# Optimization experiments

Measured on AMD Instinct MI355X. Metric: run time of the kernel, lower is better.

Reference implementation:

```python
import jax, jax.numpy as jnp
import numpy as np

N_NEIGHBORS = 16
N_CLASSES = 10

def setup_inputs() -> dict:
    key = jax.random.key(0)
    k1, k2, k3 = jax.random.split(key, 3)
    x = jax.random.normal(k1, (1024, 64), dtype=jnp.float32)
    train_data = jax.random.normal(k2, (100000, 64), dtype=jnp.float32)
    train_labels = jax.random.randint(k3, (100000,), 0, N_CLASSES, dtype=jnp.int64)
    return {"x": x, "train_data": train_data, "train_labels": train_labels}

def reference(x, train_data, train_labels):
    # Pairwise L2 distances [B, N] via the quadratic expansion (same math as cdist p=2)
    x2 = jnp.sum(x * x, axis=-1, keepdims=True)            # [B, 1]
    t2 = jnp.sum(train_data * train_data, axis=-1)          # [N]
    d2 = x2 - 2.0 * (x @ train_data.T) + t2                 # [B, N]
    dist = jnp.sqrt(jnp.maximum(d2, 0.0))
    # k smallest distances
    neg_d, idx = jax.lax.top_k(-dist, N_NEIGHBORS)           # [B, k]
    d = -neg_d
    labels = train_labels[idx]                               # [B, k] gather
    # weights = 'distance': inverse distance, with exact-match rows handled
    w = 1.0 / d
    inf_mask = jnp.isinf(w)
    inf_row = jnp.any(inf_mask, axis=1, keepdims=True)
    w = jnp.where(inf_row, inf_mask.astype(w.dtype), w)
    # scatter_add weighted votes into [B, C]
    B = x.shape[0]
    rows = jnp.arange(B)[:, None]
    proba = jnp.zeros((B, N_CLASSES), dtype=w.dtype).at[rows, labels].add(w)
    s = jnp.sum(proba, axis=1, keepdims=True)
    s = jnp.where(s == 0.0, jnp.float32(1.0), s)
    proba = proba / s
    return jnp.argmax(proba, axis=1), proba
```

## Files before the change

### kernel.cpp

```cpp
#include <hip/hip_runtime.h>
#include <math.h>


constexpr int D        = 64;
constexpr int K        = 16;
constexpr int NCLS     = 10;
constexpr int CHUNKLEN = 896;
constexpr int NCHUNK   = 112;
constexpr int NPAD     = NCHUNK * CHUNKLEN + 32;
constexpr int NSUB     = 64;
constexpr int SUBLEN   = 128;
constexpr int SLOT     = 16;
constexpr int MSEL     = 48;

typedef __attribute__((ext_vector_type(8))) short bf16x8_t;
typedef __attribute__((ext_vector_type(4))) float f32x4_t;
typedef unsigned short ushort_t;

__device__ __forceinline__ ushort_t f32_to_bf16_rne(float f) {
  unsigned int u = __float_as_uint(f);
  unsigned int r = u + 0x7FFFu + ((u >> 16) & 1u);
  return (ushort_t)(r >> 16);
}

__device__ __forceinline__ bf16x8_t pack_bf16x8(float4 a, float4 b) {
  union { ushort_t u[8]; bf16x8_t v; } r;
  r.u[0] = f32_to_bf16_rne(a.x); r.u[1] = f32_to_bf16_rne(a.y);
  r.u[2] = f32_to_bf16_rne(a.z); r.u[3] = f32_to_bf16_rne(a.w);
  r.u[4] = f32_to_bf16_rne(b.x); r.u[5] = f32_to_bf16_rne(b.y);
  r.u[6] = f32_to_bf16_rne(b.z); r.u[7] = f32_to_bf16_rne(b.w);
  return r.v;
}

__global__ __launch_bounds__(256) void cvt_train(
    const float* __restrict__ t, ushort_t* __restrict__ tb,
    float* __restrict__ t2, float* __restrict__ nt2h, int N)
{
  int gid = blockIdx.x * 256 + threadIdx.x;
  int row = gid >> 2, qt = gid & 3;
  if (row >= NPAD) return;
  ushort_t* dst = tb + (size_t)row * D + qt * 16;
  if (row >= N) {
    uint2 z = make_uint2(0u, 0u);
    #pragma unroll
    for (int i = 0; i < 4; ++i) *reinterpret_cast<uint2*>(dst + i * 4) = z;
    if (qt == 0) { t2[row] = INFINITY; nt2h[row] = -INFINITY; }
    return;
  }
  const float* src = t + (size_t)row * D + qt * 16;
  float nrm = 0.f;
  #pragma unroll
  for (int i = 0; i < 4; ++i) {
    float4 v = *reinterpret_cast<const float4*>(src + i * 4);
    nrm = fmaf(v.x, v.x, nrm); nrm = fmaf(v.y, v.y, nrm);
    nrm = fmaf(v.z, v.z, nrm); nrm = fmaf(v.w, v.w, nrm);
    uint2 hh = make_uint2(
      (unsigned)f32_to_bf16_rne(v.x) | ((unsigned)f32_to_bf16_rne(v.y) << 16),
      (unsigned)f32_to_bf16_rne(v.z) | ((unsigned)f32_to_bf16_rne(v.w) << 16));
    *reinterpret_cast<uint2*>(dst + i * 4) = hh;
  }
  nrm += __shfl_xor(nrm, 1);
  nrm += __shfl_xor(nrm, 2);
  if (qt == 0) { t2[row] = nrm; nt2h[row] = -0.5f * nrm; }
}

__global__ __launch_bounds__(256) void knn_sample(
    const ushort_t* __restrict__ tb, const float* __restrict__ x,
    const float* __restrict__ nt2h, float* __restrict__ samp)
{
  const int tid = threadIdx.x;
  const int w = tid >> 6, lane = tid & 63;
  const int lh = lane & 15, lg = lane >> 4;
  const int qb = blockIdx.x, sub = blockIdx.y;
  const int q = qb * 64 + w * 16 + lh;

  const float* xrp = x + (size_t)q * D + lg * 8;
  bf16x8_t B0 = pack_bf16x8(*reinterpret_cast<const float4*>(xrp),
                            *reinterpret_cast<const float4*>(xrp + 4));
  bf16x8_t B1 = pack_bf16x8(*reinterpret_cast<const float4*>(xrp + 32),
                            *reinterpret_cast<const float4*>(xrp + 36));

  float Ld[4] = {-INFINITY, -INFINITY, -INFINITY, -INFINITY};

  const int pstart = sub * SUBLEN;
  const ushort_t* abase = tb + (size_t)pstart * D + lh * D + lg * 8;
  const float* nbase = nt2h + pstart + lg * 4;

  bf16x8_t A0[4], A1[4]; float4 NH[4];
  #pragma unroll
  for (int j = 0; j < 4; ++j) {
    const ushort_t* ap = abase + (size_t)j * 16 * D;
    A0[j] = *reinterpret_cast<const bf16x8_t*>(ap);
    A1[j] = *reinterpret_cast<const bf16x8_t*>(ap + 32);
    NH[j] = *reinterpret_cast<const float4*>(nbase + j * 16);
  }
  bf16x8_t N0[4], N1[4]; float4 NN[4];
  #pragma unroll
  for (int j = 0; j < 4; ++j) {
    const ushort_t* ap = abase + (size_t)(4 + j) * 16 * D;
    N0[j] = *reinterpret_cast<const bf16x8_t*>(ap);
    N1[j] = *reinterpret_cast<const bf16x8_t*>(ap + 32);
    NN[j] = *reinterpret_cast<const float4*>(nbase + (4 + j) * 16);
  }

  #pragma unroll
  for (int j = 0; j < 4; ++j) {
    f32x4_t c = {NH[j].x, NH[j].y, NH[j].z, NH[j].w};
    c = __builtin_amdgcn_mfma_f32_16x16x32_bf16(A0[j], B0, c, 0, 0, 0);
    c = __builtin_amdgcn_mfma_f32_16x16x32_bf16(A1[j], B1, c, 0, 0, 0);
    #pragma unroll
    for (int r = 0; r < 4; ++r) {
      float sv = c[r];
      if (sv > Ld[3]) {
        Ld[3] = sv;
        if (Ld[3] > Ld[2]) { float s_ = Ld[3]; Ld[3] = Ld[2]; Ld[2] = s_; }
        if (Ld[2] > Ld[1]) { float s_ = Ld[2]; Ld[2] = Ld[1]; Ld[1] = s_; }
        if (Ld[1] > Ld[0]) { float s_ = Ld[1]; Ld[1] = Ld[0]; Ld[0] = s_; }
      }
    }
  }
  #pragma unroll
  for (int j = 0; j < 4; ++j) {
    f32x4_t c = {NN[j].x, NN[j].y, NN[j].z, NN[j].w};
    c = __builtin_amdgcn_mfma_f32_16x16x32_bf16(N0[j], B0, c, 0, 0, 0);
    c = __builtin_amdgcn_mfma_f32_16x16x32_bf16(N1[j], B1, c, 0, 0, 0);
    #pragma unroll
    for (int r = 0; r < 4; ++r) {
      float sv = c[r];
      if (sv > Ld[3]) {
        Ld[3] = sv;
        if (Ld[3] > Ld[2]) { float s_ = Ld[3]; Ld[3] = Ld[2]; Ld[2] = s_; }
        if (Ld[2] > Ld[1]) { float s_ = Ld[2]; Ld[2] = Ld[1]; Ld[1] = s_; }
        if (Ld[1] > Ld[0]) { float s_ = Ld[1]; Ld[1] = Ld[0]; Ld[0] = s_; }
      }
    }
  }

  float* outp = samp + (size_t)q * (NSUB * 16) + sub * 16 + lg * 4;
  *reinterpret_cast<float4*>(outp) = make_float4(Ld[0], Ld[1], Ld[2], Ld[3]);
}

__global__ __launch_bounds__(256) void knn_theta(
    const float* __restrict__ samp, float* __restrict__ theta, int B)
{
  const int w = threadIdx.x >> 6, lane = threadIdx.x & 63;
  const int q = blockIdx.x * 4 + w;
  if (q >= B) return;

  const float* s = samp + (size_t)q * (NSUB * 16) + lane * 16;
  float4 p0 = *reinterpret_cast<const float4*>(s);
  float4 p1 = *reinterpret_cast<const float4*>(s + 4);
  float4 p2 = *reinterpret_cast<const float4*>(s + 8);
  float4 p3 = *reinterpret_cast<const float4*>(s + 12);
  float L0[4] = {p0.x, p0.y, p0.z, p0.w};
  float L1[4] = {p1.x, p1.y, p1.z, p1.w};
  float L2[4] = {p2.x, p2.y, p2.z, p2.w};
  float L3[4] = {p3.x, p3.y, p3.z, p3.w};

  float th = -INFINITY;
  for (int r = 0; r < K; ++r) {
    float bd = fmaxf(fmaxf(L0[0], L1[0]), fmaxf(L2[0], L3[0]));
    #pragma unroll
    for (int sdx = 0; sdx < 6; ++sdx) bd = fmaxf(bd, __shfl_xor(bd, 32 >> sdx));
    if (L0[0] == bd) { L0[0] = L0[1]; L0[1] = L0[2]; L0[2] = L0[3]; L0[3] = -INFINITY; }
    if (L1[0] == bd) { L1[0] = L1[1]; L1[1] = L1[2]; L1[2] = L1[3]; L1[3] = -INFINITY; }
    if (L2[0] == bd) { L2[0] = L2[1]; L2[1] = L2[2]; L2[2] = L2[3]; L2[3] = -INFINITY; }
    if (L3[0] == bd) { L3[0] = L3[1]; L3[1] = L3[2]; L3[2] = L3[3]; L3[3] = -INFINITY; }
    th = bd;
  }
  if (lane == 0) theta[q] = th;
}

__global__ __launch_bounds__(256) void knn_filter(
    const ushort_t* __restrict__ tb, const float* __restrict__ x,
    const float* __restrict__ nt2h, const float* __restrict__ theta,
    int* __restrict__ cnts, int2* __restrict__ cand2)
{
  __shared__ int  cnt_l[64];
  __shared__ int2 list_p[64][SLOT];

  const int tid = threadIdx.x;
  const int w = tid >> 6, lane = tid & 63;
  const int lh = lane & 15, lg = lane >> 4;

  const int d   = blockIdx.x + 16 * blockIdx.y;
  const int xcd = d & 7;
  const int t_  = d >> 3;
  const int qb  = t_ & 15;
  const int ch  = ((t_ >> 4) << 3) | xcd;

  const int q0 = qb * 64;
  const int wp0 = ch * CHUNKLEN + w * (CHUNKLEN / 4);

  if (tid < 64) cnt_l[tid] = 0;
  __syncthreads();

  bf16x8_t Bq0[4], Bq1[4];
  float th[4];
  #pragma unroll
  for (int ct = 0; ct < 4; ++ct) {
    const float* xrp = x + (size_t)(q0 + ct * 16 + lh) * D + lg * 8;
    Bq0[ct] = pack_bf16x8(*reinterpret_cast<const float4*>(xrp),
                          *reinterpret_cast<const float4*>(xrp + 4));
    Bq1[ct] = pack_bf16x8(*reinterpret_cast<const float4*>(xrp + 32),
                          *reinterpret_cast<const float4*>(xrp + 36));
    th[ct] = theta[q0 + ct * 16 + lh];
  }

  const ushort_t* abase = tb + (size_t)wp0 * D + lh * D + lg * 8;
  const float* nbase = nt2h + wp0 + lg * 4;

  bf16x8_t cA0 = *reinterpret_cast<const bf16x8_t*>(abase);
  bf16x8_t cA1 = *reinterpret_cast<const bf16x8_t*>(abase + 32);
  float4   cNA = *reinterpret_cast<const float4*>(nbase);
  bf16x8_t cB0 = *reinterpret_cast<const bf16x8_t*>(abase + (size_t)16 * D);
  bf16x8_t cB1 = *reinterpret_cast<const bf16x8_t*>(abase + (size_t)16 * D + 32);
  float4   cNB = *reinterpret_cast<const float4*>(nbase + 16);

  #define PROCESS(A0_, A1_, NH_, GIDX_)                                           \
    {                                                                             \
      const int pg = wp0 + (GIDX_) * 16 + lg * 4;                                 \
      _Pragma("unroll")                                                           \
      for (int ct = 0; ct < 4; ++ct) {                                            \
        f32x4_t c = {NH_.x, NH_.y, NH_.z, NH_.w};                                 \
        c = __builtin_amdgcn_mfma_f32_16x16x32_bf16(A0_, Bq0[ct], c, 0, 0, 0);    \
        c = __builtin_amdgcn_mfma_f32_16x16x32_bf16(A1_, Bq1[ct], c, 0, 0, 0);    \
        unsigned m = (c[0] >= th[ct] ? 1u : 0u) | (c[1] >= th[ct] ? 2u : 0u)      \
                   | (c[2] >= th[ct] ? 4u : 0u) | (c[3] >= th[ct] ? 8u : 0u);     \
        if (m) {                                                                  \
          const int qloc = ct * 16 + lh;                                          \
          int n = __popc(m);                                                      \
          int base = atomicAdd(&cnt_l[qloc], n);                                  \
          while (m) {                                                             \
            int r = __ffs(m) - 1; m &= m - 1;                                     \
            float sv = (r == 0) ? c[0] : (r == 1) ? c[1] : (r == 2) ? c[2] : c[3];\
            if (base < SLOT)                                                      \
              list_p[qloc][base] = make_int2(pg + r, __float_as_int(sv));         \
            ++base;                                                               \
          }                                                                       \
        }                                                                         \
      }                                                                           \
    }

  for (int g = 0; g < 7; ++g) {
    const ushort_t* an = abase + (size_t)(2 * g + 2) * 16 * D;
    bf16x8_t nA0 = *reinterpret_cast<const bf16x8_t*>(an);
    bf16x8_t nA1 = *reinterpret_cast<const bf16x8_t*>(an + 32);
    float4   nNA = *reinterpret_cast<const float4*>(nbase + (2 * g + 2) * 16);
    bf16x8_t nB0 = *reinterpret_cast<const bf16x8_t*>(an + (size_t)16 * D);
    bf16x8_t nB1 = *reinterpret_cast<const bf16x8_t*>(an + (size_t)16 * D + 32);
    float4   nNB = *reinterpret_cast<const float4*>(nbase + (2 * g + 3) * 16);

    PROCESS(cA0, cA1, cNA, 2 * g);
    PROCESS(cB0, cB1, cNB, 2 * g + 1);

    cA0 = nA0; cA1 = nA1; cNA = nNA;
    cB0 = nB0; cB1 = nB1; cNB = nNB;
  }
  #undef PROCESS

  __syncthreads();
  if (tid < 64) {
    int n = cnt_l[tid]; if (n > SLOT) n = SLOT;
    size_t o = (size_t)(q0 + tid) * NCHUNK + ch;
    cnts[o] = n;
    for (int j = 0; j < n; ++j) cand2[o * SLOT + j] = list_p[tid][j];
  }
}

__global__ __launch_bounds__(256) void knn_vote(
    const float* __restrict__ x, const float* __restrict__ train,
    const float* __restrict__ t2, const int* __restrict__ labels,
    const int* __restrict__ cnts, const int2* __restrict__ cand2,
    float* __restrict__ out, int B, int N)
{
  __shared__ int2  cpair[NCHUNK * SLOT];
  __shared__ float sortd[MSEL];
  __shared__ int   sorti[MSEL];
  __shared__ float xs[D];
  __shared__ int   total_s;
  __shared__ float x2_s;

  const int tid = threadIdx.x;
  const int w = tid >> 6, lane = tid & 63;
  const int q = blockIdx.x;

  if (tid == 0) total_s = 0;
  if (tid < D) xs[tid] = x[(size_t)q * D + tid];
  if (tid < MSEL) { sortd[tid] = INFINITY; sorti[tid] = 0x7fffffff; }
  __syncthreads();

  if (w == 0) {
    float v = xs[lane];
    float s = v * v;
    #pragma unroll
    for (int o = 32; o > 0; o >>= 1) s += __shfl_xor(s, o);
    if (lane == 0) x2_s = s;
  }
  if (tid < NCHUNK) {
    int n = cnts[(size_t)q * NCHUNK + tid];
    int base = atomicAdd(&total_s, n);
    const int2* src = cand2 + ((size_t)q * NCHUNK + tid) * SLOT;
    for (int j = 0; j < n; ++j) cpair[base + j] = src[j];
  }
  __syncthreads();

  const int total = total_s;
  const float x2 = x2_s;

  for (int j = tid; j < total; j += 256) {
    int2 mine = cpair[j];
    float ms = __int_as_float(mine.y);
    int   mi = mine.x;
    int rank = 0;
    for (int k = 0; k < total; ++k) {
      int2 o = cpair[k];
      float os = __int_as_float(o.y);
      rank += (os > ms || (os == ms && o.x < mi)) ? 1 : 0;
    }
    if (rank < MSEL) { sortd[rank] = ms; sorti[rank] = mi; }
  }
  __syncthreads();

  if (tid < MSEL) {
    int idx = sorti[tid];
    float d2v = INFINITY;
    if (idx != 0x7fffffff) {
      const float* tr = train + (size_t)idx * D;
      float dot = 0.f;
      #pragma unroll
      for (int i = 0; i < 16; ++i) {
        float4 tv = *reinterpret_cast<const float4*>(tr + i * 4);
        dot = fmaf(xs[i * 4 + 0], tv.x, dot); dot = fmaf(xs[i * 4 + 1], tv.y, dot);
        dot = fmaf(xs[i * 4 + 2], tv.z, dot); dot = fmaf(xs[i * 4 + 3], tv.w, dot);
      }
      d2v = fmaxf(x2 - 2.f * dot + t2[idx], 0.f);
    }
    sortd[tid] = d2v;
  }
  __syncthreads();

  if (w == 0) {
    float vd = (lane < MSEL) ? sortd[lane] : INFINITY;
    int   vi = (lane < MSEL) ? sorti[lane] : 0x7fffffff;
    float myD = INFINITY; int myI = 0;
    for (int r = 0; r < K; ++r) {
      float bd = vd; int bi = vi;
      #pragma unroll
      for (int s = 0; s < 6; ++s) {
        int off = 32 >> s;
        float od = __shfl_xor(bd, off);
        int   oi = __shfl_xor(bi, off);
        if (od < bd || (od == bd && oi < bi)) { bd = od; bi = oi; }
      }
      if (vd == bd && vi == bi) { vd = INFINITY; vi = 0x7fffffff; }
      if (lane == r) { myD = bd; myI = bi; }
    }

    int valid = (lane < K) && (myD < INFINITY) && (myI < N);
    float dist = sqrtf(fmaxf(myD, 0.f));
    int lab = labels[(valid && myI < N) ? myI : 0];
    int isz = (valid && dist == 0.f) ? 1 : 0;
    float wgt = 1.f / dist;

    float accw[NCLS]; float acci[NCLS]; int anyInf = 0;
    #pragma unroll
    for (int c = 0; c < NCLS; ++c) { accw[c] = 0.f; acci[c] = 0.f; }
    for (int r = 0; r < K; ++r) {
      int   vr   = __shfl(valid, r);
      int   labr = __shfl(lab, r);
      float wgtr = __shfl(wgt, r);
      int   iszr = __shfl(isz, r);
      if (vr) {
        anyInf |= iszr;
        #pragma unroll
        for (int c = 0; c < NCLS; ++c) {
          accw[c] += (labr == c) ? wgtr : 0.f;
          acci[c] += (labr == c && iszr) ? 1.f : 0.f;
        }
      }
    }

    if (lane == 0) {
      float proba[NCLS]; float s = 0.f;
      #pragma unroll
      for (int c = 0; c < NCLS; ++c) { proba[c] = anyInf ? acci[c] : accw[c]; s += proba[c]; }
      if (s == 0.f) s = 1.f;
      #pragma unroll
      for (int c = 0; c < NCLS; ++c) proba[c] = proba[c] / s;
      int best = 0; float bv = proba[0];
      #pragma unroll
      for (int c = 1; c < NCLS; ++c) if (proba[c] > bv) { bv = proba[c]; best = c; }
      out[q] = (float)best;
      #pragma unroll
      for (int c = 0; c < NCLS; ++c) out[B + q * NCLS + c] = proba[c];
    }
  }
}

extern "C" void kernel_launch(void* const* d_in, const int* in_sizes, int n_in,
                              void* d_out, int out_size, void* d_ws, size_t ws_size,
                              hipStream_t stream)
{
  const float* x      = (const float*)d_in[0];
  const float* train  = (const float*)d_in[1];
  const int*   labels = (const int*)d_in[2];
  float* out = (float*)d_out;

  const int B = in_sizes[0] / D;
  const int N = in_sizes[2];

  char* ws = (char*)d_ws;
  size_t off = 0;
  ushort_t* train_bf = (ushort_t*)(ws + off); off += (size_t)NPAD * D * 2;
  float*    t2       = (float*)(ws + off);    off += (size_t)NPAD * 4;
  float*    nt2h     = (float*)(ws + off);    off += (size_t)NPAD * 4;
  float*    theta    = (float*)(ws + off);    off += (size_t)B * 4;
  int*      cnts     = (int*)(ws + off);      off += (size_t)B * NCHUNK * 4;
  int2*     cand2    = (int2*)(ws + off);     off += (size_t)B * NCHUNK * SLOT * 8;
  float*    samp     = (float*)cand2;

  cvt_train<<<(NPAD * 4 + 255) / 256, 256, 0, stream>>>(train, train_bf, t2, nt2h, N);
  knn_sample<<<dim3(B / 64, NSUB), 256, 0, stream>>>(train_bf, x, nt2h, samp);
  knn_theta<<<(B + 3) / 4, 256, 0, stream>>>(samp, theta, B);
  knn_filter<<<dim3(16, NCHUNK), 256, 0, stream>>>(train_bf, x, nt2h, theta, cnts, cand2);
  knn_vote<<<B, 256, 0, stream>>>(x, train, t2, labels, cnts, cand2, out, B, N);
}
```

Baseline: 116.8 us.

## Simplify candidate filtering, unroll rank loop, split rescoring dot across lanes

In the scan kernel, the per-element threshold bitmask is replaced by a max-of-four early test followed by per-element atomicAdd insertion, making the common no-hit path cheaper at the cost of more atomics on hits. The vote kernel pads the candidate list to a multiple of four with sentinel entries and unrolls the rank-counting loop by four, which raises instruction-level parallelism. The exact fp32 rescoring of the 48 selected candidates now spreads each 64-element dot product over four lanes and combines them with shuffles, so each thread does less serial work.

```diff
diff --git a/kernel.cpp b/kernel.cpp
--- a/kernel.cpp
+++ b/kernel.cpp
@@ -219,24 +219,22 @@
 
   #define PROCESS(A0_, A1_, NH_, GIDX_)                                           \
     {                                                                             \
-      const int pg = wp0 + (GIDX_) * 16 + lg * 4;                                 \
       _Pragma("unroll")                                                           \
       for (int ct = 0; ct < 4; ++ct) {                                            \
         f32x4_t c = {NH_.x, NH_.y, NH_.z, NH_.w};                                 \
         c = __builtin_amdgcn_mfma_f32_16x16x32_bf16(A0_, Bq0[ct], c, 0, 0, 0);    \
         c = __builtin_amdgcn_mfma_f32_16x16x32_bf16(A1_, Bq1[ct], c, 0, 0, 0);    \
-        unsigned m = (c[0] >= th[ct] ? 1u : 0u) | (c[1] >= th[ct] ? 2u : 0u)      \
-                   | (c[2] >= th[ct] ? 4u : 0u) | (c[3] >= th[ct] ? 8u : 0u);     \
-        if (m) {                                                                  \
+        float mx = fmaxf(fmaxf(c[0], c[1]), fmaxf(c[2], c[3]));                   \
+        if (mx >= th[ct]) {                         \
           const int qloc = ct * 16 + lh;                                          \
-          int n = __popc(m);                                                      \
-          int base = atomicAdd(&cnt_l[qloc], n);                                  \
-          while (m) {                                                             \
-            int r = __ffs(m) - 1; m &= m - 1;                                     \
-            float sv = (r == 0) ? c[0] : (r == 1) ? c[1] : (r == 2) ? c[2] : c[3];\
-            if (base < SLOT)                                                      \
-              list_p[qloc][base] = make_int2(pg + r, __float_as_int(sv));         \
-            ++base;                                                               \
+          const int pg = wp0 + (GIDX_) * 16 + lg * 4;                             \
+          _Pragma("unroll")                                                       \
+          for (int r = 0; r < 4; ++r) {                                           \
+            if (c[r] >= th[ct]) {                                                 \
+              int pos = atomicAdd(&cnt_l[qloc], 1);                               \
+              if (pos < SLOT)                                                     \
+                list_p[qloc][pos] = make_int2(pg + r, __float_as_int(c[r]));      \
+            }                                                                     \
           }                                                                       \
         }                                                                         \
       }                                                                           \
@@ -274,7 +272,7 @@
     const int* __restrict__ cnts, const int2* __restrict__ cand2,
     float* __restrict__ out, int B, int N)
 {
-  __shared__ int2  cpair[NCHUNK * SLOT];
+  __shared__ int2  cpair[NCHUNK * SLOT + 4];
   __shared__ float sortd[MSEL];
   __shared__ int   sorti[MSEL];
   __shared__ float xs[D];
@@ -306,37 +304,51 @@
   __syncthreads();
 
   const int total = total_s;
+  const int totalPad = (total + 3) & ~3;
   const float x2 = x2_s;
+  if (tid < totalPad - total)
+    cpair[total + tid] = make_int2(0x7fffffff, __float_as_int(-INFINITY));
+  __syncthreads();
 
   for (int j = tid; j < total; j += 256) {
     int2 mine = cpair[j];
     float ms = __int_as_float(mine.y);
     int   mi = mine.x;
     int rank = 0;
-    for (int k = 0; k < total; ++k) {
-      int2 o = cpair[k];
-      float os = __int_as_float(o.y);
-      rank += (os > ms || (os == ms && o.x < mi)) ? 1 : 0;
+    for (int k = 0; k < totalPad; k += 4) {
+      int2 o0 = cpair[k];     int2 o1 = cpair[k + 1];
+      int2 o2 = cpair[k + 2]; int2 o3 = cpair[k + 3];
+      float s0 = __int_as_float(o0.y), s1 = __int_as_float(o1.y);
+      float s2 = __int_as_float(o2.y), s3 = __int_as_float(o3.y);
+      rank += ((s0 > ms || (s0 == ms && o0.x < mi)) ? 1 : 0)
+            + ((s1 > ms || (s1 == ms && o1.x < mi)) ? 1 : 0)
+            + ((s2 > ms || (s2 == ms && o2.x < mi)) ? 1 : 0)
+            + ((s3 > ms || (s3 == ms && o3.x < mi)) ? 1 : 0);
     }
     if (rank < MSEL) { sortd[rank] = ms; sorti[rank] = mi; }
   }
   __syncthreads();
 
-  if (tid < MSEL) {
-    int idx = sorti[tid];
-    float d2v = INFINITY;
+  if (tid < MSEL * 4) {
+    const int ci = tid >> 2, qt = tid & 3;
+    const int idx = sorti[ci];
+    float dot = 0.f;
     if (idx != 0x7fffffff) {
-      const float* tr = train + (size_t)idx * D;
-      float dot = 0.f;
-      #pragma unroll
-      for (int i = 0; i < 16; ++i) {
+      const float* tr = train + (size_t)idx * D + qt * 16;
+      #pragma unroll
+      for (int i = 0; i < 4; ++i) {
         float4 tv = *reinterpret_cast<const float4*>(tr + i * 4);
-        dot = fmaf(xs[i * 4 + 0], tv.x, dot); dot = fmaf(xs[i * 4 + 1], tv.y, dot);
-        dot = fmaf(xs[i * 4 + 2], tv.z, dot); dot = fmaf(xs[i * 4 + 3], tv.w, dot);
+        dot = fmaf(xs[qt * 16 + i * 4 + 0], tv.x, dot);
+        dot = fmaf(xs[qt * 16 + i * 4 + 1], tv.y, dot);
+        dot = fmaf(xs[qt * 16 + i * 4 + 2], tv.z, dot);
+        dot = fmaf(xs[qt * 16 + i * 4 + 3], tv.w, dot);
       }
-      d2v = fmaxf(x2 - 2.f * dot + t2[idx], 0.f);
-    }
-    sortd[tid] = d2v;
+    }
+    dot += __shfl_xor(dot, 1);
+    dot += __shfl_xor(dot, 2);
+    if (qt == 0)
+      sortd[ci] = (idx != 0x7fffffff)
+                ? fmaxf(x2 - 2.f * dot + t2[idx], 0.f) : INFINITY;
   }
   __syncthreads();
 
```

New measurement: 116.9 us. No clear change (+0.0%).
